# Optimization experiments

Measured on AMD Instinct MI355X. Metric: run time of the kernel, lower is better.

The kernel has to match this reference:

```python
import jax, jax.numpy as jnp
import numpy as np

# static video/block geometry (matches grid_sizes = [12, 30, 50], block_layout = (3, 5, 10))
F_, H_, W_ = 12, 30, 50
FB, HB, WB = 3, 5, 10
P1, P2, P3 = F_ // FB, H_ // HB, W_ // WB      # (4, 6, 5) -> 120 tokens per block
NB = FB * HB * WB                               # 150 blocks
B = 1
N = F_ * H_ * W_                                # 18000 tokens
DIM, NH = 1536, 12
HD = DIM // NH                                  # 128
CC = HD // 2                                    # 64 rotary pairs
SPLITS = (CC - 2 * (CC // 3), CC // 3, CC // 3) # (22, 21, 21) per torch split
EPS = 1e-6
MAXP = max(F_, H_, W_)


def _block_weight():
    # BlockDistanceConv3D with transform='linear': 1 - d/dmax, column-normalized (sum over dim=0)
    f, i, j = np.meshgrid(np.arange(FB), np.arange(HB), np.arange(WB), indexing='ij')
    centers = np.stack([f.ravel() + 0.5, i.ravel() + 0.5, j.ravel() + 0.5], 1).astype(np.float64)
    d = np.linalg.norm(centers[:, None] - centers[None, :], axis=-1)
    mat = 1.0 - d / d.max()
    mat = mat / mat.sum(axis=0, keepdims=True)
    return jnp.asarray(mat, jnp.float32)        # [NB, NB]

W_BLK = _block_weight()


def setup_inputs():
    key = jax.random.key(0)
    ks = jax.random.split(key, 10)
    x = jax.random.normal(ks[0], (B, N, DIM), jnp.float32)
    seq_lens = jnp.full((B,), N, jnp.int32)
    grid_sizes = jnp.tile(jnp.array([[F_, H_, W_]], jnp.int32), (B, 1))
    # rope freqs table [MAXP, CC]: per-axis sub-tables of widths SPLITS, base 1e4
    cols = []
    for sz in SPLITS:
        inv = 1.0 / (10000.0 ** (np.arange(sz, dtype=np.float64) / sz))
        cols.append(np.arange(MAXP)[:, None] * inv[None, :])
    ang = np.concatenate(cols, axis=1)
    freqs_cos = jnp.asarray(np.cos(ang), jnp.float32)
    freqs_sin = jnp.asarray(np.sin(ang), jnp.float32)
    s = 0.02
    wq = jax.random.normal(ks[1], (DIM, DIM), jnp.float32) * s
    wk = jax.random.normal(ks[2], (DIM, DIM), jnp.float32) * s
    wv = jax.random.normal(ks[3], (DIM, DIM), jnp.float32) * s
    wo = jax.random.normal(ks[4], (DIM, DIM), jnp.float32) * s
    bq = jax.random.normal(ks[5], (DIM,), jnp.float32) * 0.01
    bk = jax.random.normal(ks[6], (DIM,), jnp.float32) * 0.01
    bv = jax.random.normal(ks[7], (DIM,), jnp.float32) * 0.01
    bo = jnp.zeros((DIM,), jnp.float32)
    nq_w = 1.0 + 0.1 * jax.random.normal(ks[8], (DIM,), jnp.float32)
    nk_w = 1.0 + 0.1 * jax.random.normal(ks[9], (DIM,), jnp.float32)
    return dict(x=x, seq_lens=seq_lens, grid_sizes=grid_sizes,
                freqs_cos=freqs_cos, freqs_sin=freqs_sin,
                wq=wq, bq=bq, wk=wk, bk=bk, wv=wv, bv=bv, wo=wo, bo=bo,
                nq_w=nq_w, nk_w=nk_w)


def _rmsnorm(t, w):
    return t * jax.lax.rsqrt(jnp.mean(t * t, -1, keepdims=True) + EPS) * w


def _pos_tab(tab):
    # expand per-axis freq table into per-token table [N, CC] (f-major, then h, then w)
    c0, c1 = SPLITS[0], SPLITS[0] + SPLITS[1]
    f = jnp.broadcast_to(tab[:F_, :c0][:, None, None, :], (F_, H_, W_, SPLITS[0]))
    h = jnp.broadcast_to(tab[:H_, c0:c1][None, :, None, :], (F_, H_, W_, SPLITS[1]))
    w = jnp.broadcast_to(tab[:W_, c1:][None, None, :, :], (F_, H_, W_, SPLITS[2]))
    return jnp.concatenate([f, h, w], -1).reshape(N, CC)


def _rope(t, cos, sin):
    # complex multiply on interleaved pairs, real arithmetic: (x0+ix1)*(c+is)
    tr = t.reshape(B, N, NH, CC, 2)
    x0, x1 = tr[..., 0], tr[..., 1]
    c = cos[None, :, None, :]
    s = sin[None, :, None, :]
    return jnp.stack([x0 * c - x1 * s, x0 * s + x1 * c], -1).reshape(B, N, NH, HD)


def _to_blocks(t):
    # 'b (fb p1 hb p2 wb p3) h d -> (b h) (fb hb wb) (p1 p2 p3) d'
    t = t.reshape(B, FB, P1, HB, P2, WB, P3, NH, HD)
    t = t.transpose(0, 7, 1, 3, 5, 2, 4, 6, 8)
    return t.reshape(B * NH, NB, P1 * P2 * P3, HD)


def reference(x, seq_lens, grid_sizes, freqs_cos, freqs_sin,
              wq, bq, wk, bk, wv, bv, wo, bo, nq_w, nk_w):
    # qkv projections (float32 throughout, as torch upcasts q/k/v to float)
    q = x @ wq.T + bq
    k = x @ wk.T + bk
    v = x @ wv.T + bv
    # RMSNorm over full dim, then relu + eps (linear-attention positivity)
    q = jax.nn.relu(_rmsnorm(q, nq_w)) + EPS
    k = jax.nn.relu(_rmsnorm(k, nk_w)) + EPS
    q = q.reshape(B, N, NH, HD)
    k = k.reshape(B, N, NH, HD)
    v = v.reshape(B, N, NH, HD)
    pc, ps = _pos_tab(freqs_cos), _pos_tab(freqs_sin)
    q_rope = _rope(q, pc, ps)
    k_rope = _rope(k, pc, ps)
    qb, kb, vb, qrb, krb = map(_to_blocks, (q, k, v, q_rope, k_rope))
    # per-block linear attention state: kv[b,n] = k_rope^T @ v
    kv = jnp.einsum('bnpd,bnpe->bnde', krb, vb)           # [B*NH, NB, HD, HD]
    kv = jnp.einsum('oi,bide->bode', W_BLK, kv)            # block-distance mixing (1x1 conv)
    # normalizer: block_mix(q @ sum_p k)
    ksum = kb.sum(axis=2)                                  # [B*NH, NB, HD]
    qk = jnp.einsum('bnpd,bnd->bnp', qb, ksum)             # [B*NH, NB, P]
    norm = jnp.einsum('oi,bip->bop', W_BLK, qk)[..., None] + EPS
    out = jnp.einsum('bnpd,bnde->bnpe', qrb, kv) / norm    # [B*NH, NB, P, HD]
    # '(b h) n p d -> b (fb p1 hb p2 wb p3) (h d)'
    out = out.reshape(B, NH, FB, HB, WB, P1, P2, P3, HD)
    out = out.transpose(0, 2, 5, 3, 6, 4, 7, 1, 8).reshape(B, N, DIM)
    return out @ wo.T + bo
```

## Files before the change

kernel.cpp:

```cpp
#include <hip/hip_runtime.h>
#include <stdint.h>


typedef unsigned short u16;
typedef unsigned int   u32;

typedef _Float16 f16x8 __attribute__((ext_vector_type(8)));
typedef float    f32x4 __attribute__((ext_vector_type(4)));

#define N_TOK 18000
#define MPAD  18048
#define DIMD  1536
#define NHH   12
#define HD    128
#define CCH   64
#define QKVN  4608
#define NBLK  150
#define PBLK  120
#define EPSF  1e-6f

#define DEVFN static __device__ __forceinline__
#define AS1 __attribute__((address_space(1)))
#define AS3 __attribute__((address_space(3)))

DEVFN u16 f2h(float f){ _Float16 h = (_Float16)f; return __builtin_bit_cast(u16, h); }
DEVFN float h2f(u16 u){ _Float16 h = __builtin_bit_cast(_Float16, u); return (float)h; }
DEVFN int2 pack4h(float a,float b,float c,float d){
  int2 r;
  r.x = (int)((u32)f2h(a) | ((u32)f2h(b)<<16));
  r.y = (int)((u32)f2h(c) | ((u32)f2h(d)<<16));
  return r;
}
DEVFN int4 packi4(float4 lo4, float4 hi4){
  int2 lo = pack4h(lo4.x, lo4.y, lo4.z, lo4.w);
  int2 hi = pack4h(hi4.x, hi4.y, hi4.z, hi4.w);
  int4 r; r.x=lo.x; r.y=lo.y; r.z=hi.x; r.w=hi.y;
  return r;
}

DEVFN void gl_lds16(const u16* g, u16* l){
  __builtin_amdgcn_global_load_lds((const AS1 void*)g, (AS3 void*)l, 16, 0, 0);
}

DEVFN int tok_of(int b, int p){
  int fb = b/50, hb = (b/10)%5, wb = b%10;
  int p1 = p/30; int pr = p - p1*30; int p2 = pr/5, p3 = pr - p2*5;
  return (fb*4 + p1)*1500 + (hb*6 + p2)*50 + (wb*5 + p3);
}
DEVFN void tok_pos(int b, int p, int& tok, int& f, int& h2, int& w2){
  int fb = b/50, hb = (b/10)%5, wb = b%10;
  int p1 = p/30; int pr = p - p1*30; int p2 = pr/5, p3 = pr - p2*5;
  f = fb*4 + p1; h2 = hb*6 + p2; w2 = wb*5 + p3;
  tok = (f*30 + h2)*50 + w2;
}


__global__ void conv_x_k(const float* __restrict__ x, u16* __restrict__ xh){
  const long i = ((long)blockIdx.x*256 + threadIdx.x)*8;
  if (i >= (long)MPAD*DIMD) return;
  if (i < (long)N_TOK*DIMD){
    const float4 a = *(const float4*)(x + i);
    const float4 b = *(const float4*)(x + i + 4);
    *(int4*)(xh + i) = packi4(a, b);
  } else {
    *(int4*)(xh + i) = make_int4(0,0,0,0);
  }
}

__global__ void conv_w_k(const float* __restrict__ wq, const float* __restrict__ wk,
                         const float* __restrict__ wv, const float* __restrict__ wo,
                         const float* __restrict__ bq, const float* __restrict__ bk,
                         const float* __restrict__ bv,
                         u16* __restrict__ wqkvb, u16* __restrict__ wob, float* __restrict__ bqkv){
  const long i = (long)blockIdx.x*256 + threadIdx.x;
  const long idx = i*4;
  const long SQ = (long)DIMD*DIMD;
  const long WQKV = 3*SQ;
  if (idx < WQKV){
    const float* src = (idx < SQ) ? (wq + idx) : (idx < 2*SQ ? wk + (idx - SQ) : wv + (idx - 2*SQ));
    const float4 v = *(const float4*)src;
    *(int2*)(wqkvb + idx) = pack4h(v.x, v.y, v.z, v.w);
  } else if (idx < WQKV + SQ){
    const long j = idx - WQKV;
    const float4 v = *(const float4*)(wo + j);
    *(int2*)(wob + j) = pack4h(v.x, v.y, v.z, v.w);
  }
  if (i < 3*DIMD) bqkv[i] = (i < DIMD) ? bq[i] : (i < 2*DIMD ? bk[i - DIMD] : bv[i - 2*DIMD]);
}

__global__ void wblk_k(float* __restrict__ wblk, u16* __restrict__ wh){
  __shared__ double cs[NBLK];
  const int t = threadIdx.x;
  const double dmax = sqrt(101.0);
  if (t < NBLK){
    const int fi = t/50, hi = (t/10)%5, wi = t%10;
    double s = 0.0;
    for (int o = 0; o < NBLK; o++){
      const int fo = o/50, ho = (o/10)%5, wo = o%10;
      const int df = fo-fi, dh = ho-hi, dw = wo-wi;
      s += 1.0 - sqrt((double)(df*df + dh*dh + dw*dw))/dmax;
    }
    cs[t] = s;
  }
  __syncthreads();
  for (int idx = t; idx < NBLK*NBLK; idx += 256){
    const int o = idx/NBLK, i = idx%NBLK;
    const int fo = o/50, ho = (o/10)%5, wo = o%10;
    const int fi = i/50, hi = (i/10)%5, wi = i%10;
    const int df = fo-fi, dh = ho-hi, dw = wo-wi;
    const double v = 1.0 - sqrt((double)(df*df + dh*dh + dw*dw))/dmax;
    wblk[idx] = (float)(v / cs[i]);
  }
  for (int idx = t; idx < 160*160; idx += 256){
    const int o = idx/160, i = idx%160;
    u16 hv = 0;
    if (o < NBLK && i < NBLK){
      const int fo = o/50, ho = (o/10)%5, wo = o%10;
      const int fi = i/50, hi = (i/10)%5, wi = i%10;
      const int df = fo-fi, dh = ho-hi, dw = wo-wi;
      const double v = 1.0 - sqrt((double)(df*df + dh*dh + dw*dw))/dmax;
      hv = f2h((float)(v / cs[i]));
    }
    wh[idx] = hv;
  }
}

__global__ __launch_bounds__(256) void gemm_qkv(const u16* __restrict__ A, const u16* __restrict__ B,
                                                const float* __restrict__ bias,
                                                u16* __restrict__ qb, u16* __restrict__ kb, u16* __restrict__ vb){
  __shared__ u16 As[128*32];
  __shared__ u16 Bs[128*32];
  const int t = threadIdx.x;
  const int bn = blockIdx.x, bm = blockIdx.y;
  const long row0 = (long)bm*128; const int gcol0 = bn*128;
  const int K = DIMD;
  const int wave = t>>6, lane = t&63, lr = lane&15, quad = lane>>4;
  const int wm = (wave&1)*64, wn = (wave>>1)*64;
  f32x4 acc[4][4] = {};

  const int c0 = t, c1 = t + 256;
  const u16* ga0 = A + (row0 + (c0>>2))*K + (c0&3)*8;
  const u16* ga1 = A + (row0 + (c1>>2))*K + (c1&3)*8;
  const u16* gb0 = B + (long)(gcol0 + (c0>>2))*K + (c0&3)*8;
  const u16* gb1 = B + (long)(gcol0 + (c1>>2))*K + (c1&3)*8;
  u16* la0 = As + c0*8; u16* la1 = As + c1*8;
  u16* lb0 = Bs + c0*8; u16* lb1 = Bs + c1*8;

  for (int k0 = 0; k0 < K; k0 += 32){
    gl_lds16(ga0 + k0, la0); gl_lds16(ga1 + k0, la1);
    gl_lds16(gb0 + k0, lb0); gl_lds16(gb1 + k0, lb1);
    __syncthreads();
    const f16x8* As8 = (const f16x8*)As;
    const f16x8* Bs8 = (const f16x8*)Bs;
    f16x8 aF[4], bF[4];
#pragma unroll
    for (int mt = 0; mt < 4; mt++) aF[mt] = As8[(wm + mt*16 + lr)*4 + quad];
#pragma unroll
    for (int nt = 0; nt < 4; nt++) bF[nt] = Bs8[(wn + nt*16 + lr)*4 + quad];
#pragma unroll
    for (int mt = 0; mt < 4; mt++)
#pragma unroll
      for (int nt = 0; nt < 4; nt++)
        acc[mt][nt] = __builtin_amdgcn_mfma_f32_16x16x32_f16(aF[mt], bF[nt], acc[mt][nt], 0, 0, 0);
    __syncthreads();
  }

  const int which = bn/12;
  u16* dst = (which == 0) ? qb : (which == 1 ? kb : vb);
  const int col0l = (bn - which*12)*128;
#pragma unroll
  for (int mt = 0; mt < 4; mt++)
#pragma unroll
    for (int nt = 0; nt < 4; nt++){
      const int gcolb = gcol0 + wn + nt*16 + lr;
      const float bb = bias[gcolb];
      const int colb = col0l + wn + nt*16 + lr;
#pragma unroll
      for (int r = 0; r < 4; r++){
        const long rr = row0 + wm + mt*16 + quad*4 + r;
        if (rr < N_TOK) dst[rr*DIMD + colb] = f2h(acc[mt][nt][r] + bb);
      }
    }
}

__global__ __launch_bounds__(256) void gemm_bt(const u16* __restrict__ A, const u16* __restrict__ B,
                                               const float* __restrict__ bias, float* __restrict__ C, int K){
  __shared__ u16 As[128*32];
  __shared__ u16 Bs[128*32];
  const int t = threadIdx.x;
  const int bn = blockIdx.x, bm = blockIdx.y;
  const long row0 = (long)bm*128; const int col0 = bn*128;
  const int wave = t>>6, lane = t&63, lr = lane&15, quad = lane>>4;
  const int wm = (wave&1)*64, wn = (wave>>1)*64;
  f32x4 acc[4][4] = {};

  const int c0 = t, c1 = t + 256;
  const u16* ga0 = A + (row0 + (c0>>2))*K + (c0&3)*8;
  const u16* ga1 = A + (row0 + (c1>>2))*K + (c1&3)*8;
  const u16* gb0 = B + (long)(col0 + (c0>>2))*K + (c0&3)*8;
  const u16* gb1 = B + (long)(col0 + (c1>>2))*K + (c1&3)*8;
  u16* la0 = As + c0*8; u16* la1 = As + c1*8;
  u16* lb0 = Bs + c0*8; u16* lb1 = Bs + c1*8;

  for (int k0 = 0; k0 < K; k0 += 32){
    gl_lds16(ga0 + k0, la0); gl_lds16(ga1 + k0, la1);
    gl_lds16(gb0 + k0, lb0); gl_lds16(gb1 + k0, lb1);
    __syncthreads();
    const f16x8* As8 = (const f16x8*)As;
    const f16x8* Bs8 = (const f16x8*)Bs;
    f16x8 aF[4], bF[4];
#pragma unroll
    for (int mt = 0; mt < 4; mt++) aF[mt] = As8[(wm + mt*16 + lr)*4 + quad];
#pragma unroll
    for (int nt = 0; nt < 4; nt++) bF[nt] = Bs8[(wn + nt*16 + lr)*4 + quad];
#pragma unroll
    for (int mt = 0; mt < 4; mt++)
#pragma unroll
      for (int nt = 0; nt < 4; nt++)
        acc[mt][nt] = __builtin_amdgcn_mfma_f32_16x16x32_f16(aF[mt], bF[nt], acc[mt][nt], 0, 0, 0);
    __syncthreads();
  }
#pragma unroll
  for (int mt = 0; mt < 4; mt++)
#pragma unroll
    for (int nt = 0; nt < 4; nt++){
      const int colb = col0 + wn + nt*16 + lr;
      const float bb = bias[colb];
#pragma unroll
      for (int r = 0; r < 4; r++){
        const long rr = row0 + wm + mt*16 + quad*4 + r;
        if (rr < N_TOK) C[rr*DIMD + colb] = acc[mt][nt][r] + bb;
      }
    }
}

__global__ __launch_bounds__(256) void norm_k(u16* __restrict__ qb, u16* __restrict__ kb,
                                              const float* __restrict__ nqw, const float* __restrict__ nkw){
  __shared__ float red[4];
  __shared__ float s_scale;
  const int n = blockIdx.x, t = threadIdx.x, lane = t&63, wv = t>>6;
  u16* bufs[2]; bufs[0] = qb; bufs[1] = kb;
  const float* wgts[2]; wgts[0] = nqw; wgts[1] = nkw;
  for (int pass = 0; pass < 2; pass++){
    u16* row = bufs[pass] + (long)n*DIMD;
    const float* wgt = wgts[pass];
    float v[6];
    float ssq = 0.f;
#pragma unroll
    for (int i = 0; i < 6; i++){ v[i] = h2f(row[t + i*256]); ssq += v[i]*v[i]; }
#pragma unroll
    for (int o = 32; o > 0; o >>= 1) ssq += __shfl_down(ssq, o);
    if (lane == 0) red[wv] = ssq;
    __syncthreads();
    if (t == 0) s_scale = rsqrtf((red[0]+red[1]+red[2]+red[3])/(float)DIMD + EPSF);
    __syncthreads();
    const float sc = s_scale;
#pragma unroll
    for (int i = 0; i < 6; i++){
      float r = fmaxf(v[i]*sc*wgt[t + i*256], 0.f) + EPSF;
      row[t + i*256] = f2h(r);
    }
    __syncthreads();
  }
}

__global__ __launch_bounds__(128) void ksum_k(const u16* __restrict__ kb, float* __restrict__ ksum){
  const int hb = blockIdx.x; const int h = hb/NBLK, b = hb%NBLK; const int d = threadIdx.x;
  float s = 0.f;
  for (int p = 0; p < PBLK; p++)
    s += h2f(kb[(long)tok_of(b, p)*DIMD + h*HD + d]);
  ksum[(long)hb*HD + d] = s;
}

__global__ __launch_bounds__(128) void qk_k(const u16* __restrict__ qb, const float* __restrict__ ksum,
                                            float* __restrict__ qk){
  __shared__ float ks[HD];
  const int hb = blockIdx.x, h = hb/NBLK, b = hb%NBLK, t = threadIdx.x;
  ks[t] = ksum[(long)hb*HD + t];
  __syncthreads();
  if (t < PBLK){
    const u16* row = qb + (long)tok_of(b, t)*DIMD + h*HD;
    float s = 0.f;
#pragma unroll
    for (int d8 = 0; d8 < 16; d8++){
      int4 v4 = *(const int4*)(row + d8*8);
      const u16* pv = (const u16*)&v4;
#pragma unroll
      for (int j = 0; j < 8; j++) s += h2f(pv[j])*ks[d8*8 + j];
    }
    qk[(long)hb*PBLK + t] = s;
  }
}

__global__ __launch_bounds__(128) void mixqk_k(const float* __restrict__ qk, const float* __restrict__ wblk,
                                               float* __restrict__ nrm){
  const int ho = blockIdx.x, h = ho/NBLK, o = ho%NBLK, t = threadIdx.x;
  if (t >= PBLK) return;
  float s = 0.f;
  for (int i = 0; i < NBLK; i++) s += wblk[o*NBLK + i]*qk[((long)h*NBLK + i)*PBLK + t];
  nrm[(long)ho*PBLK + t] = s + EPSF;
}

__global__ __launch_bounds__(256) void kv_k(const u16* __restrict__ kb, const u16* __restrict__ vb,
                                            const float* __restrict__ fcos, const float* __restrict__ fsin,
                                            u16* __restrict__ kv1){
  __shared__ u16 Ap[4][128][32];
  __shared__ u16 Bp[4][128][32];
  const int hb = blockIdx.x, h = hb/NBLK, b = hb%NBLK, t = threadIdx.x;
  for (int idx = t; idx < 128*64; idx += 256){
    const int p = idx>>6, cc = idx&63;
    u16 v0=0, v1=0, r0=0, r1=0;
    if (p < PBLK){
      int tok, f, hh, ww; tok_pos(b, p, tok, f, hh, ww);
      const long tb = (long)tok*DIMD + h*HD + 2*cc;
      const u32 vv = *(const u32*)&vb[tb];
      const u32 kk = *(const u32*)&kb[tb];
      const int pos = (cc < 22) ? f : (cc < 43 ? hh : ww);
      const float cv = fcos[pos*CCH + cc], sv = fsin[pos*CCH + cc];
      const float x0 = h2f((u16)kk), x1 = h2f((u16)(kk>>16));
      v0 = (u16)vv; v1 = (u16)(vv>>16);
      r0 = f2h(x0*cv - x1*sv); r1 = f2h(x0*sv + x1*cv);
    }
    const int kp = p>>5, j = p&31;
    Ap[kp][2*cc][j] = v0; Ap[kp][2*cc+1][j] = v1;
    Bp[kp][2*cc][j] = r0; Bp[kp][2*cc+1][j] = r1;
  }
  __syncthreads();
  const int wave = t>>6, lane = t&63, lr = lane&15, quad = lane>>4;
  const int wm = (wave&1)*64, wn = (wave>>1)*64;
  f32x4 acc[4][4] = {};
#pragma unroll
  for (int kp = 0; kp < 4; kp++){
    f16x8 aF[4], bF[4];
#pragma unroll
    for (int mt = 0; mt < 4; mt++) aF[mt] = *(const f16x8*)&Ap[kp][wm + mt*16 + lr][quad*8];
#pragma unroll
    for (int nt = 0; nt < 4; nt++) bF[nt] = *(const f16x8*)&Bp[kp][wn + nt*16 + lr][quad*8];
#pragma unroll
    for (int mt = 0; mt < 4; mt++)
#pragma unroll
      for (int nt = 0; nt < 4; nt++)
        acc[mt][nt] = __builtin_amdgcn_mfma_f32_16x16x32_f16(aF[mt], bF[nt], acc[mt][nt], 0, 0, 0);
  }
  u16* outp = kv1 + (long)hb*HD*HD;
#pragma unroll
  for (int mt = 0; mt < 4; mt++)
#pragma unroll
    for (int nt = 0; nt < 4; nt++)
#pragma unroll
      for (int r = 0; r < 4; r++)
        outp[(wm + mt*16 + quad*4 + r)*HD + wn + nt*16 + lr] = f2h(acc[mt][nt][r]);
}

__global__ __launch_bounds__(256) void mix_gemm(const u16* __restrict__ kv1, const u16* __restrict__ wh,
                                                u16* __restrict__ kv2){
  __shared__ u16 Xs[5][128][32];
  const int h = blockIdx.y, jc = blockIdx.x, t = threadIdx.x;
  const long base = (long)h*NBLK*HD*HD + jc*128;
#pragma unroll
  for (int it = 0; it < 10; it++){
    const int idx = t + it*256;
    const int i = idx>>4, jg = idx&15;
    int4 v = make_int4(0,0,0,0);
    if (i < NBLK) v = *(const int4*)&kv1[base + (long)i*HD*HD + jg*8];
    const u16* pv = (const u16*)&v;
    const int kp = i>>5, il = i&31;
    const int ib = ((((il>>3) ^ jg) & 3)<<3) | (il&7);
#pragma unroll
    for (int e = 0; e < 8; e++) Xs[kp][jg*8 + e][ib] = pv[e];
  }
  __syncthreads();
  const int wave = t>>6, lane = t&63, lr = lane&15, quad = lane>>4;
  const int wm = (wave&1)*80, wn = (wave>>1)*64;
  f32x4 acc[5][4] = {};
#pragma unroll
  for (int kp = 0; kp < 5; kp++){
    f16x8 aF[5], bF[4];
#pragma unroll
    for (int mt = 0; mt < 5; mt++)
      aF[mt] = *(const f16x8*)&wh[(wm + mt*16 + lr)*160 + kp*32 + quad*8];
#pragma unroll
    for (int nt = 0; nt < 4; nt++){
      const int j = wn + nt*16 + lr;
      bF[nt] = *(const f16x8*)&Xs[kp][j][((quad ^ (j>>3)) & 3)<<3];
    }
#pragma unroll
    for (int mt = 0; mt < 5; mt++)
#pragma unroll
      for (int nt = 0; nt < 4; nt++)
        acc[mt][nt] = __builtin_amdgcn_mfma_f32_16x16x32_f16(aF[mt], bF[nt], acc[mt][nt], 0, 0, 0);
  }
#pragma unroll
  for (int mt = 0; mt < 5; mt++)
#pragma unroll
    for (int nt = 0; nt < 4; nt++)
#pragma unroll
      for (int r = 0; r < 4; r++){
        const int o = wm + mt*16 + quad*4 + r;
        if (o < NBLK)
          kv2[(long)(h*NBLK + o)*HD*HD + jc*128 + wn + nt*16 + lr] = f2h(acc[mt][nt][r]);
      }
}

__global__ __launch_bounds__(256) void attn_k(const u16* __restrict__ qb, const u16* __restrict__ kv2,
                                              const float* __restrict__ fcos, const float* __restrict__ fsin,
                                              const float* __restrict__ nrm, u16* __restrict__ aout){
  __shared__ u16 Ap[4][128][32];
  __shared__ u16 Bp[4][128][32];
  const int ho = blockIdx.x, h = ho/NBLK, o = ho%NBLK, t = threadIdx.x;
  for (int idx = t; idx < 128*64; idx += 256){
    const int p = idx>>6, cc = idx&63;
    u32 w = 0;
    if (p < PBLK){
      int tok, f, hh, ww; tok_pos(o, p, tok, f, hh, ww);
      const u32 qq = *(const u32*)&qb[(long)tok*DIMD + h*HD + 2*cc];
      const int pos = (cc < 22) ? f : (cc < 43 ? hh : ww);
      const float cv = fcos[pos*CCH + cc], sv = fsin[pos*CCH + cc];
      const float x0 = h2f((u16)qq), x1 = h2f((u16)(qq>>16));
      w = (u32)f2h(x0*cv - x1*sv) | ((u32)f2h(x0*sv + x1*cv) << 16);
    }
    *(u32*)&Ap[(2*cc)>>5][p][(2*cc)&31] = w;
  }
  const u16* kv2p = kv2 + (long)ho*HD*HD;
  for (int idx = t; idx < 128*16; idx += 256){
    const int e = idx>>4, d8 = (idx&15)*8;
    int4 vv = *(const int4*)&kv2p[e*HD + d8];
    *(int4*)&Bp[d8>>5][e][d8&31] = vv;
  }
  __syncthreads();
  const int wave = t>>6, lane = t&63, lr = lane&15, quad = lane>>4;
  const int wm = (wave&1)*64, wn = (wave>>1)*64;
  f32x4 acc[4][4] = {};
#pragma unroll
  for (int kp = 0; kp < 4; kp++){
    f16x8 aF[4], bF[4];
#pragma unroll
    for (int mt = 0; mt < 4; mt++) aF[mt] = *(const f16x8*)&Ap[kp][wm + mt*16 + lr][quad*8];
#pragma unroll
    for (int nt = 0; nt < 4; nt++) bF[nt] = *(const f16x8*)&Bp[kp][wn + nt*16 + lr][quad*8];
#pragma unroll
    for (int mt = 0; mt < 4; mt++)
#pragma unroll
      for (int nt = 0; nt < 4; nt++)
        acc[mt][nt] = __builtin_amdgcn_mfma_f32_16x16x32_f16(aF[mt], bF[nt], acc[mt][nt], 0, 0, 0);
  }
#pragma unroll
  for (int mt = 0; mt < 4; mt++)
#pragma unroll
    for (int r = 0; r < 4; r++){
      const int p = wm + mt*16 + quad*4 + r;
      if (p >= PBLK) continue;
      const float inv = 1.0f / nrm[(long)ho*PBLK + p];
      const long tb = (long)tok_of(o, p)*DIMD + h*HD;
#pragma unroll
      for (int nt = 0; nt < 4; nt++)
        aout[tb + wn + nt*16 + lr] = f2h(acc[mt][nt][r]*inv);
    }
}

extern "C" void kernel_launch(void* const* d_in, const int* in_sizes, int n_in,
                              void* d_out, int out_size, void* d_ws, size_t ws_size,
                              hipStream_t stream){
  const float* x    = (const float*)d_in[0];
  const float* fcos = (const float*)d_in[3];
  const float* fsin = (const float*)d_in[4];
  const float* wq   = (const float*)d_in[5];
  const float* bq   = (const float*)d_in[6];
  const float* wk   = (const float*)d_in[7];
  const float* bk   = (const float*)d_in[8];
  const float* wv   = (const float*)d_in[9];
  const float* bv   = (const float*)d_in[10];
  const float* wo   = (const float*)d_in[11];
  const float* bo   = (const float*)d_in[12];
  const float* nqw  = (const float*)d_in[13];
  const float* nkw  = (const float*)d_in[14];
  float* out = (float*)d_out;
  (void)in_sizes; (void)n_in; (void)out_size; (void)ws_size;

  char* ws = (char*)d_ws; size_t off = 0;
  auto alloc = [&](size_t b)->void*{ void* p = ws + off; off += (b + 255) & ~(size_t)255; return p; };
  const size_t SQ = (size_t)DIMD*DIMD;
  u16*   wqkvb = (u16*)  alloc(3*SQ*2);
  u16*   wob   = (u16*)  alloc(SQ*2);
  float* bqkv  = (float*)alloc((size_t)3*DIMD*4);
  float* wblk  = (float*)alloc((size_t)NBLK*NBLK*4);
  u16*   wh    = (u16*)  alloc((size_t)160*160*2);
  u16*   qb    = (u16*)  alloc((size_t)MPAD*DIMD*2);
  u16*   kb    = (u16*)  alloc((size_t)MPAD*DIMD*2);
  u16*   vb    = (u16*)  alloc((size_t)MPAD*DIMD*2);
  u16*   kv1   = (u16*)  alloc((size_t)NHH*NBLK*HD*HD*2);
  float* ksum  = (float*)alloc((size_t)NHH*NBLK*HD*4);
  float* qk    = (float*)alloc((size_t)NHH*NBLK*PBLK*4);
  float* nrm   = (float*)alloc((size_t)NHH*NBLK*PBLK*4);
  u16*   kv2   = kb;
  u16*   xh    = kv1;

  conv_w_k<<<9216, 256, 0, stream>>>(wq, wk, wv, wo, bq, bk, bv, wqkvb, wob, bqkv);
  wblk_k<<<1, 256, 0, stream>>>(wblk, wh);
  conv_x_k<<<(MPAD*DIMD/8 + 255)/256, 256, 0, stream>>>(x, xh);
  gemm_qkv<<<dim3(QKVN/128, MPAD/128), 256, 0, stream>>>(xh, wqkvb, bqkv, qb, kb, vb);
  norm_k<<<N_TOK, 256, 0, stream>>>(qb, kb, nqw, nkw);
  ksum_k<<<NHH*NBLK, 128, 0, stream>>>(kb, ksum);
  qk_k<<<NHH*NBLK, 128, 0, stream>>>(qb, ksum, qk);
  mixqk_k<<<NHH*NBLK, 128, 0, stream>>>(qk, wblk, nrm);
  kv_k<<<NHH*NBLK, 256, 0, stream>>>(kb, vb, fcos, fsin, kv1);
  mix_gemm<<<dim3(HD*HD/128, NHH), 256, 0, stream>>>(kv1, wh, kv2);
  attn_k<<<NHH*NBLK, 256, 0, stream>>>(qb, kv2, fcos, fsin, nrm, qb);
  gemm_bt<<<dim3(DIMD/128, MPAD/128), 256, 0, stream>>>(qb, wob, bo, out, DIMD);
}
```

Baseline: 1.099 ms.

## Replace 128x128 GEMMs with pipelined 256x256 double-buffered swizzled MFMA kernel

```diff
diff --git a/kernel.cpp b/kernel.cpp
--- a/kernel.cpp
+++ b/kernel.cpp
@@ -9,7 +9,7 @@
 typedef float    f32x4 __attribute__((ext_vector_type(4)));
 
 #define N_TOK 18000
-#define MPAD  18048
+#define MPAD  18176
 #define DIMD  1536
 #define NHH   12
 #define HD    128
@@ -40,6 +40,10 @@
 
 DEVFN void gl_lds16(const u16* g, u16* l){
   __builtin_amdgcn_global_load_lds((const AS1 void*)g, (AS3 void*)l, 16, 0, 0);
+}
+
+DEVFN f32x4 mf(f16x8 a, f16x8 b, f32x4 c){
+  return __builtin_amdgcn_mfma_f32_16x16x32_f16(a, b, c, 0, 0, 0);
 }
 
 DEVFN int tok_of(int b, int p){
@@ -125,113 +129,136 @@
   }
 }
 
-__global__ __launch_bounds__(256) void gemm_qkv(const u16* __restrict__ A, const u16* __restrict__ B,
-                                                const float* __restrict__ bias,
-                                                u16* __restrict__ qb, u16* __restrict__ kb, u16* __restrict__ vb){
-  __shared__ u16 As[128*32];
-  __shared__ u16 Bs[128*32];
+
+#define STG_A(bB, kt, h) { const int ko_ = (kt)*64 + (h)*32; \
+  gl_lds16(Aat + offA0 + ko_, lds + (bB)*32768 + (h)*8192 + t*8); \
+  gl_lds16(Aat + offA1 + ko_, lds + (bB)*32768 + (h)*8192 + t*8 + 4096); }
+#define STG_B(bB, kt, h) { const int ko_ = (kt)*64 + (h)*32; \
+  gl_lds16(Bat + offB0 + ko_, lds + (bB)*32768 + 16384 + (h)*8192 + t*8); \
+  gl_lds16(Bat + offB1 + ko_, lds + (bB)*32768 + 16384 + (h)*8192 + t*8 + 4096); }
+#define VMC(n) asm volatile("s_waitcnt vmcnt(" #n ")" ::: "memory")
+#define BARR() __builtin_amdgcn_s_barrier()
+#define LGK0() asm volatile("s_waitcnt lgkmcnt(0)" ::: "memory")
+
+#define PH_ODD(bB, kk, STG) { \
+  const u16* ab_ = lds + (bB)*32768 + (kk)*8192 + arow; \
+  const u16* bb_ = lds + (bB)*32768 + 16384 + (kk)*8192 + brow; \
+  _Pragma("unroll") for (int mt_=0; mt_<8; mt_++) aF[mt_] = *(const f16x8*)(ab_ + mt_*512); \
+  bF[0] = *(const f16x8*)(bb_); bF[1] = *(const f16x8*)(bb_ + 512); \
+  STG; BARR(); LGK0(); \
+  __builtin_amdgcn_s_setprio(1); \
+  _Pragma("unroll") for (int mt_=0; mt_<8; mt_++){ \
+    acc[mt_][0] = mf(aF[mt_], bF[0], acc[mt_][0]); \
+    acc[mt_][1] = mf(aF[mt_], bF[1], acc[mt_][1]); } \
+  __builtin_amdgcn_s_setprio(0); BARR(); }
+
+#define PH_EVEN(bB, kk, STG) { \
+  const u16* bb_ = lds + (bB)*32768 + 16384 + (kk)*8192 + brow; \
+  bF[2] = *(const f16x8*)(bb_ + 1024); bF[3] = *(const f16x8*)(bb_ + 1536); \
+  STG; BARR(); LGK0(); \
+  __builtin_amdgcn_s_setprio(1); \
+  _Pragma("unroll") for (int mt_=0; mt_<8; mt_++){ \
+    acc[mt_][2] = mf(aF[mt_], bF[2], acc[mt_][2]); \
+    acc[mt_][3] = mf(aF[mt_], bF[3], acc[mt_][3]); } \
+  __builtin_amdgcn_s_setprio(0); BARR(); }
+
+DEVFN void gemm256_core(const u16* __restrict__ Aat, const u16* __restrict__ Bat,
+                        u16* lds, long row0, long col0, int K, f32x4 (&acc)[8][4]){
   const int t = threadIdx.x;
+  const int lane = t&63, lr = lane&15, q = lane>>4;
+  const int w = t>>6, wr = w>>2, wc = w&3;
+  const int slot8 = (q ^ ((lr>>1)&3))*8;
+  const int arow = (wr*128 + lr)*32 + slot8;
+  const int brow = (wc*64 + lr)*32 + slot8;
+  const int s1 = t + 512;
+  const int r0 = t>>2, r1 = s1>>2;
+  const int g0 = ((t&3)  ^ ((r0>>1)&3))*8;
+  const int g1 = ((s1&3) ^ ((r1>>1)&3))*8;
+  const long offA0 = (row0 + r0)*(long)K + g0, offA1 = (row0 + r1)*(long)K + g1;
+  const long offB0 = (col0 + r0)*(long)K + g0, offB1 = (col0 + r1)*(long)K + g1;
+
+  f16x8 aF[8], bF[4];
+  STG_A(0,0,0); STG_B(0,0,0); STG_A(0,0,1); STG_B(0,0,1);
+  STG_A(1,1,0); STG_B(1,1,0); STG_A(1,1,1);
+  VMC(6); BARR();
+
+  const int NIT = K/128;
+#pragma unroll 1
+  for (int j = 0; j < NIT-1; ++j){
+    const int c1 = 2*j+1, p0 = 2*j+2, p1 = 2*j+3;
+    PH_ODD (0,0, STG_B(1,c1,1));
+    PH_EVEN(0,0, STG_A(0,p0,0));
+    PH_ODD (0,1, STG_B(0,p0,0));
+    PH_EVEN(0,1, { STG_A(0,p0,1); VMC(6); });
+    PH_ODD (1,0, STG_B(0,p0,1));
+    PH_EVEN(1,0, STG_A(1,p1,0));
+    PH_ODD (1,1, STG_B(1,p1,0));
+    PH_EVEN(1,1, { STG_A(1,p1,1); VMC(6); });
+  }
+  { const int c1 = 2*(K/128)-1;
+    PH_ODD (0,0, STG_B(1,c1,1));
+    PH_EVEN(0,0, );
+    PH_ODD (0,1, );
+    PH_EVEN(0,1, VMC(0));
+    PH_ODD (1,0, );
+    PH_EVEN(1,0, );
+    PH_ODD (1,1, );
+    PH_EVEN(1,1, );
+  }
+}
+
+__global__ __launch_bounds__(512, 2) void gemm_qkv256(const u16* __restrict__ A, const u16* __restrict__ B,
+                                                      const float* __restrict__ bias,
+                                                      u16* __restrict__ qb, u16* __restrict__ kb,
+                                                      u16* __restrict__ vb){
+  __shared__ u16 lds[65536];
   const int bn = blockIdx.x, bm = blockIdx.y;
-  const long row0 = (long)bm*128; const int gcol0 = bn*128;
-  const int K = DIMD;
-  const int wave = t>>6, lane = t&63, lr = lane&15, quad = lane>>4;
-  const int wm = (wave&1)*64, wn = (wave>>1)*64;
-  f32x4 acc[4][4] = {};
-
-  const int c0 = t, c1 = t + 256;
-  const u16* ga0 = A + (row0 + (c0>>2))*K + (c0&3)*8;
-  const u16* ga1 = A + (row0 + (c1>>2))*K + (c1&3)*8;
-  const u16* gb0 = B + (long)(gcol0 + (c0>>2))*K + (c0&3)*8;
-  const u16* gb1 = B + (long)(gcol0 + (c1>>2))*K + (c1&3)*8;
-  u16* la0 = As + c0*8; u16* la1 = As + c1*8;
-  u16* lb0 = Bs + c0*8; u16* lb1 = Bs + c1*8;
-
-  for (int k0 = 0; k0 < K; k0 += 32){
-    gl_lds16(ga0 + k0, la0); gl_lds16(ga1 + k0, la1);
-    gl_lds16(gb0 + k0, lb0); gl_lds16(gb1 + k0, lb1);
-    __syncthreads();
-    const f16x8* As8 = (const f16x8*)As;
-    const f16x8* Bs8 = (const f16x8*)Bs;
-    f16x8 aF[4], bF[4];
-#pragma unroll
-    for (int mt = 0; mt < 4; mt++) aF[mt] = As8[(wm + mt*16 + lr)*4 + quad];
-#pragma unroll
-    for (int nt = 0; nt < 4; nt++) bF[nt] = Bs8[(wn + nt*16 + lr)*4 + quad];
-#pragma unroll
-    for (int mt = 0; mt < 4; mt++)
-#pragma unroll
-      for (int nt = 0; nt < 4; nt++)
-        acc[mt][nt] = __builtin_amdgcn_mfma_f32_16x16x32_f16(aF[mt], bF[nt], acc[mt][nt], 0, 0, 0);
-    __syncthreads();
-  }
-
-  const int which = bn/12;
+  const long row0 = (long)bm*256, col0 = (long)bn*256;
+  f32x4 acc[8][4] = {};
+  gemm256_core(A, B, lds, row0, col0, DIMD, acc);
+
+  const int t = threadIdx.x, lane = t&63, lr = lane&15, q = lane>>4;
+  const int w = t>>6, wr = w>>2, wc = w&3;
+  const int which = bn/6;
   u16* dst = (which == 0) ? qb : (which == 1 ? kb : vb);
-  const int col0l = (bn - which*12)*128;
-#pragma unroll
-  for (int mt = 0; mt < 4; mt++)
-#pragma unroll
-    for (int nt = 0; nt < 4; nt++){
-      const int gcolb = gcol0 + wn + nt*16 + lr;
-      const float bb = bias[gcolb];
-      const int colb = col0l + wn + nt*16 + lr;
+  const int lcol0 = (bn - which*6)*256 + wc*64;
+  const int gcol0 = bn*256 + wc*64;
+#pragma unroll
+  for (int nt = 0; nt < 4; nt++){
+    const float bb = bias[gcol0 + nt*16 + lr];
+    const int col = lcol0 + nt*16 + lr;
+#pragma unroll
+    for (int mt = 0; mt < 8; mt++)
 #pragma unroll
       for (int r = 0; r < 4; r++){
-        const long rr = row0 + wm + mt*16 + quad*4 + r;
-        if (rr < N_TOK) dst[rr*DIMD + colb] = f2h(acc[mt][nt][r] + bb);
+        const long rr = row0 + wr*128 + mt*16 + q*4 + r;
+        if (rr < N_TOK) dst[rr*DIMD + col] = f2h(acc[mt][nt][r] + bb);
       }
-    }
-}
-
-__global__ __launch_bounds__(256) void gemm_bt(const u16* __restrict__ A, const u16* __restrict__ B,
-                                               const float* __restrict__ bias, float* __restrict__ C, int K){
-  __shared__ u16 As[128*32];
-  __shared__ u16 Bs[128*32];
-  const int t = threadIdx.x;
+  }
+}
+
+__global__ __launch_bounds__(512, 2) void gemm_bt256(const u16* __restrict__ A, const u16* __restrict__ B,
+                                                     const float* __restrict__ bias, float* __restrict__ C){
+  __shared__ u16 lds[65536];
   const int bn = blockIdx.x, bm = blockIdx.y;
-  const long row0 = (long)bm*128; const int col0 = bn*128;
-  const int wave = t>>6, lane = t&63, lr = lane&15, quad = lane>>4;
-  const int wm = (wave&1)*64, wn = (wave>>1)*64;
-  f32x4 acc[4][4] = {};
-
-  const int c0 = t, c1 = t + 256;
-  const u16* ga0 = A + (row0 + (c0>>2))*K + (c0&3)*8;
-  const u16* ga1 = A + (row0 + (c1>>2))*K + (c1&3)*8;
-  const u16* gb0 = B + (long)(col0 + (c0>>2))*K + (c0&3)*8;
-  const u16* gb1 = B + (long)(col0 + (c1>>2))*K + (c1&3)*8;
-  u16* la0 = As + c0*8; u16* la1 = As + c1*8;
-  u16* lb0 = Bs + c0*8; u16* lb1 = Bs + c1*8;
-
-  for (int k0 = 0; k0 < K; k0 += 32){
-    gl_lds16(ga0 + k0, la0); gl_lds16(ga1 + k0, la1);
-    gl_lds16(gb0 + k0, lb0); gl_lds16(gb1 + k0, lb1);
-    __syncthreads();
-    const f16x8* As8 = (const f16x8*)As;
-    const f16x8* Bs8 = (const f16x8*)Bs;
-    f16x8 aF[4], bF[4];
-#pragma unroll
-    for (int mt = 0; mt < 4; mt++) aF[mt] = As8[(wm + mt*16 + lr)*4 + quad];
-#pragma unroll
-    for (int nt = 0; nt < 4; nt++) bF[nt] = Bs8[(wn + nt*16 + lr)*4 + quad];
-#pragma unroll
-    for (int mt = 0; mt < 4; mt++)
-#pragma unroll
-      for (int nt = 0; nt < 4; nt++)
-        acc[mt][nt] = __builtin_amdgcn_mfma_f32_16x16x32_f16(aF[mt], bF[nt], acc[mt][nt], 0, 0, 0);
-    __syncthreads();
-  }
-#pragma unroll
-  for (int mt = 0; mt < 4; mt++)
-#pragma unroll
-    for (int nt = 0; nt < 4; nt++){
-      const int colb = col0 + wn + nt*16 + lr;
-      const float bb = bias[colb];
+  const long row0 = (long)bm*256, col0 = (long)bn*256;
+  f32x4 acc[8][4] = {};
+  gemm256_core(A, B, lds, row0, col0, DIMD, acc);
+
+  const int t = threadIdx.x, lane = t&63, lr = lane&15, q = lane>>4;
+  const int w = t>>6, wr = w>>2, wc = w&3;
+#pragma unroll
+  for (int nt = 0; nt < 4; nt++){
+    const int col = bn*256 + wc*64 + nt*16 + lr;
+    const float bb = bias[col];
+#pragma unroll
+    for (int mt = 0; mt < 8; mt++)
 #pragma unroll
       for (int r = 0; r < 4; r++){
-        const long rr = row0 + wm + mt*16 + quad*4 + r;
-        if (rr < N_TOK) C[rr*DIMD + colb] = acc[mt][nt][r] + bb;
+        const long rr = row0 + wr*128 + mt*16 + q*4 + r;
+        if (rr < N_TOK) C[rr*DIMD + col] = acc[mt][nt][r] + bb;
       }
-    }
+  }
 }
 
 __global__ __launch_bounds__(256) void norm_k(u16* __restrict__ qb, u16* __restrict__ kb,
@@ -498,7 +525,7 @@
   conv_w_k<<<9216, 256, 0, stream>>>(wq, wk, wv, wo, bq, bk, bv, wqkvb, wob, bqkv);
   wblk_k<<<1, 256, 0, stream>>>(wblk, wh);
   conv_x_k<<<(MPAD*DIMD/8 + 255)/256, 256, 0, stream>>>(x, xh);
-  gemm_qkv<<<dim3(QKVN/128, MPAD/128), 256, 0, stream>>>(xh, wqkvb, bqkv, qb, kb, vb);
+  gemm_qkv256<<<dim3(QKVN/256, MPAD/256), 512, 0, stream>>>(xh, wqkvb, bqkv, qb, kb, vb);
   norm_k<<<N_TOK, 256, 0, stream>>>(qb, kb, nqw, nkw);
   ksum_k<<<NHH*NBLK, 128, 0, stream>>>(kb, ksum);
   qk_k<<<NHH*NBLK, 128, 0, stream>>>(qb, ksum, qk);
@@ -506,5 +533,5 @@
   kv_k<<<NHH*NBLK, 256, 0, stream>>>(kb, vb, fcos, fsin, kv1);
   mix_gemm<<<dim3(HD*HD/128, NHH), 256, 0, stream>>>(kv1, wh, kv2);
   attn_k<<<NHH*NBLK, 256, 0, stream>>>(qb, kv2, fcos, fsin, nrm, qb);
-  gemm_bt<<<dim3(DIMD/128, MPAD/128), 256, 0, stream>>>(qb, wob, bo, out, DIMD);
-}
+  gemm_bt256<<<dim3(DIMD/256, MPAD/256), 512, 0, stream>>>(qb, wob, bo, out);
+}
```

Measured after the change: 1.064 ms. 1.03x faster.
